# Kernel optimization log

Hardware: AMD Instinct MI355X
Metric: run time of the kernel (lower is better)

The kernel has to match this reference:

```python
import jax, jax.numpy as jnp
import numpy as np

B, L = 8, 1024
D_IN = 80 * 4          # input_feature_size * num_temporal_dimension_reduction_steps
CODE_DIM = 512         # code_book_size (projection dim)
NUM_CODES = 8192       # num_code_books (entries argmin'd over)


def setup_inputs() -> dict:
    key = jax.random.key(0)
    k1, k2, k3 = jax.random.split(key, 3)
    input_values = jax.random.normal(k1, (B, L, D_IN), dtype=jnp.float32)
    # all-ones mask keeps N = B*L static (jit-friendly); math identical to mask==1 selection
    mask_time_indices = jnp.ones((B, L), dtype=jnp.int32)
    # xavier_uniform for Linear weight of shape (out=CODE_DIM, in=D_IN)
    limit = float(np.sqrt(6.0 / (D_IN + CODE_DIM)))
    proj_weight = jax.random.uniform(k2, (CODE_DIM, D_IN), dtype=jnp.float32,
                                     minval=-limit, maxval=limit)
    code_book = jax.random.normal(k3, (NUM_CODES, CODE_DIM), dtype=jnp.float32)
    return {"input_values": input_values, "mask_time_indices": mask_time_indices,
            "proj_weight": proj_weight, "code_book": code_book}


def reference(input_values, mask_time_indices, proj_weight, code_book):
    D = input_values.shape[-1]
    flat = input_values.reshape(-1, D)                       # (B*L, D)
    sel = flat[mask_time_indices.reshape(-1) == 1]           # (N, D) masked tokens
    targets = sel @ proj_weight.T                            # (N, CODE_DIM)
    # squared euclidean distance via GEMM expansion: ||t||^2 - 2 t.c + ||c||^2
    t2 = jnp.sum(targets * targets, axis=-1, keepdims=True)  # (N, 1)
    c2 = jnp.sum(code_book * code_book, axis=-1)             # (NUM_CODES,)
    d2 = t2 - 2.0 * (targets @ code_book.T) + c2             # (N, NUM_CODES)
    # argmin of squared distance == argmin of euclidean norm
    return jnp.argmin(d2, axis=-1)                           # (N,)
```

## Files before the change

kernel.cpp:

```cpp
#include <hip/hip_runtime.h>


#define D_IN      320
#define CODE_DIM  512
#define NUM_CODES 8192
#define N_ROWS    8192

typedef _Float16 f16;
typedef __attribute__((ext_vector_type(4))) _Float16 f16x4;
typedef __attribute__((ext_vector_type(8))) _Float16 f16x8;
typedef __attribute__((ext_vector_type(4))) float    f32x4;

__global__ __launch_bounds__(256) void c2_kernel(const float* __restrict__ cb,
                                                 float* __restrict__ c2) {
    int wave = (blockIdx.x * blockDim.x + threadIdx.x) >> 6;
    int lane = threadIdx.x & 63;
    if (wave >= NUM_CODES) return;
    const float* row = cb + (size_t)wave * CODE_DIM;
    float s = 0.f;
#pragma unroll
    for (int i = 0; i < CODE_DIM / 64; ++i) {
        float v = row[lane + 64 * i];
        s += v * v;
    }
#pragma unroll
    for (int off = 32; off > 0; off >>= 1) s += __shfl_down(s, off, 64);
    if (lane == 0) c2[wave] = s;
}

__global__ __launch_bounds__(256) void cvt_kernel(const float* __restrict__ src,
                                                  f16* __restrict__ hi,
                                                  f16* __restrict__ lo, int n4) {
    int i = blockIdx.x * blockDim.x + threadIdx.x;
    if (i >= n4) return;
    float4 v = ((const float4*)src)[i];
    f16 h0 = (f16)v.x, h1 = (f16)v.y, h2 = (f16)v.z, h3 = (f16)v.w;
    f16x4 hv = {h0, h1, h2, h3};
    f16x4 lv = {(f16)(v.x - (float)h0), (f16)(v.y - (float)h1),
                (f16)(v.z - (float)h2), (f16)(v.w - (float)h3)};
    *(f16x4*)&hi[(size_t)i * 4] = hv;
    *(f16x4*)&lo[(size_t)i * 4] = lv;
}

#define PB_M 64
#define PB_N 64
#define PB_K 32
#define PLD  (PB_K + 4)

__global__ __launch_bounds__(256) void proj_kernel(const float* __restrict__ X,
                                                   const float* __restrict__ W,
                                                   f16* __restrict__ Thi,
                                                   f16* __restrict__ Tlo) {
    __shared__ float Xs[PB_M][PLD];
    __shared__ float Wsh[PB_N][PLD];
    const int bm = blockIdx.x;
    const int bn = blockIdx.y;
    const int tid = threadIdx.x;
    const int tx = tid & 15;
    const int ty = tid >> 4;
    float acc[4][4] = {};
    for (int kc = 0; kc < D_IN; kc += PB_K) {
#pragma unroll
        for (int it = 0; it < 2; ++it) {
            int idx = tid + 256 * it;
            int r   = idx >> 3;
            int kp  = (idx & 7) * 4;
            *(float4*)&Xs[r][kp] =
                *(const float4*)(X + (size_t)(bm * PB_M + r) * D_IN + kc + kp);
            *(float4*)&Wsh[r][kp] =
                *(const float4*)(W + (size_t)(bn * PB_N + r) * D_IN + kc + kp);
        }
        __syncthreads();
#pragma unroll
        for (int kk = 0; kk < PB_K; ++kk) {
            float a[4], b[4];
#pragma unroll
            for (int i = 0; i < 4; ++i) a[i] = Xs[ty + 16 * i][kk];
#pragma unroll
            for (int j = 0; j < 4; ++j) b[j] = Wsh[tx + 16 * j][kk];
#pragma unroll
            for (int i = 0; i < 4; ++i)
#pragma unroll
                for (int j = 0; j < 4; ++j) acc[i][j] += a[i] * b[j];
        }
        __syncthreads();
    }
#pragma unroll
    for (int i = 0; i < 4; ++i)
#pragma unroll
        for (int j = 0; j < 4; ++j) {
            size_t idx = (size_t)(bm * PB_M + ty + 16 * i) * CODE_DIM +
                         bn * PB_N + tx + 16 * j;
            float v = acc[i][j];
            f16  h = (f16)v;
            Thi[idx] = h;
            Tlo[idx] = (f16)(v - (float)h);
        }
}

#define BM 128
#define BN 128
#define BK 64

__global__ __launch_bounds__(256) void dist_mfma_kernel(
        const f16* __restrict__ Thi, const f16* __restrict__ Tlo,
        const f16* __restrict__ Chi, const f16* __restrict__ Clo,
        const float* __restrict__ c2, float2* __restrict__ part) {
    __shared__ f16 Ah[BM * BK], Al[BM * BK];
    __shared__ f16 Bh[BN * BK], Bl[BN * BK];
    __shared__ float red_v[BM][2];
    __shared__ int   red_i[BM][2];

    const int tid = threadIdx.x;
    const int l   = tid & 63;
    const int w   = tid >> 6;
    const int wr  = w >> 1;
    const int wc  = w & 1;
    const int rb  = blockIdx.y * BM;
    const int cbase = blockIdx.x * BN;

    f32x4 acc[4][4];
#pragma unroll
    for (int i = 0; i < 4; ++i)
#pragma unroll
        for (int j = 0; j < 4; ++j) acc[i][j] = (f32x4){0.f, 0.f, 0.f, 0.f};

    for (int kc = 0; kc < CODE_DIM; kc += BK) {
        __syncthreads();
#pragma unroll
        for (int it = 0; it < 4; ++it) {
            int idx = tid + 256 * it;
            int r   = idx >> 3;
            int kp  = (idx & 7) * 8;
            int db  = r * 128 + ((kp * 2) ^ ((r & 7) << 4));
            size_t ga = (size_t)(rb + r) * CODE_DIM + kc + kp;
            size_t gb = (size_t)(cbase + r) * CODE_DIM + kc + kp;
            *(uint4*)((char*)Ah + db) = *(const uint4*)(Thi + ga);
            *(uint4*)((char*)Al + db) = *(const uint4*)(Tlo + ga);
            *(uint4*)((char*)Bh + db) = *(const uint4*)(Chi + gb);
            *(uint4*)((char*)Bl + db) = *(const uint4*)(Clo + gb);
        }
        __syncthreads();
#pragma unroll
        for (int ks = 0; ks < 2; ++ks) {
            const int kb = ks * 64 + (l >> 4) * 16;
            f16x8 ah[4], al[4], bh[4], bl[4];
#pragma unroll
            for (int i = 0; i < 4; ++i) {
                int r   = wr * 64 + i * 16 + (l & 15);
                int off = r * 128 + (kb ^ ((r & 7) << 4));
                ah[i] = *(const f16x8*)((const char*)Ah + off);
                al[i] = *(const f16x8*)((const char*)Al + off);
            }
#pragma unroll
            for (int j = 0; j < 4; ++j) {
                int c   = wc * 64 + j * 16 + (l & 15);
                int off = c * 128 + (kb ^ ((c & 7) << 4));
                bh[j] = *(const f16x8*)((const char*)Bh + off);
                bl[j] = *(const f16x8*)((const char*)Bl + off);
            }
#pragma unroll
            for (int i = 0; i < 4; ++i)
#pragma unroll
                for (int j = 0; j < 4; ++j) {
                    acc[i][j] = __builtin_amdgcn_mfma_f32_16x16x32_f16(
                        ah[i], bh[j], acc[i][j], 0, 0, 0);
                    acc[i][j] = __builtin_amdgcn_mfma_f32_16x16x32_f16(
                        ah[i], bl[j], acc[i][j], 0, 0, 0);
                    acc[i][j] = __builtin_amdgcn_mfma_f32_16x16x32_f16(
                        al[i], bh[j], acc[i][j], 0, 0, 0);
                }
        }
    }

#pragma unroll
    for (int i = 0; i < 4; ++i) {
        float bvv[4];
        int   bii[4];
#pragma unroll
        for (int p = 0; p < 4; ++p) { bvv[p] = 3.4e38f; bii[p] = 0x7fffffff; }
#pragma unroll
        for (int j = 0; j < 4; ++j) {
            int   code = cbase + wc * 64 + j * 16 + (l & 15);
            float cc   = c2[code];
#pragma unroll
            for (int p = 0; p < 4; ++p) {
                float s = cc - 2.0f * acc[i][j][p];
                if (s < bvv[p]) { bvv[p] = s; bii[p] = code; }
            }
        }
#pragma unroll
        for (int off = 1; off < 16; off <<= 1) {
#pragma unroll
            for (int p = 0; p < 4; ++p) {
                float ov = __shfl_xor(bvv[p], off, 64);
                int   oi = __shfl_xor(bii[p], off, 64);
                if (ov < bvv[p] || (ov == bvv[p] && oi < bii[p])) {
                    bvv[p] = ov; bii[p] = oi;
                }
            }
        }
        if ((l & 15) == 0) {
#pragma unroll
            for (int p = 0; p < 4; ++p) {
                int rloc = wr * 64 + i * 16 + (l >> 4) * 4 + p;
                red_v[rloc][wc] = bvv[p];
                red_i[rloc][wc] = bii[p];
            }
        }
    }
    __syncthreads();
    if (tid < BM) {
        float v0 = red_v[tid][0], v1 = red_v[tid][1];
        int   i0 = red_i[tid][0], i1 = red_i[tid][1];
        bool  t1 = (v1 < v0) || (v1 == v0 && i1 < i0);
        part[(size_t)(rb + tid) * (NUM_CODES / BN) + blockIdx.x] =
            make_float2(t1 ? v1 : v0, __int_as_float(t1 ? i1 : i0));
    }
}

__global__ __launch_bounds__(256) void argmin_reduce_kernel(
        const float2* __restrict__ part, int* __restrict__ out) {
    int row  = blockIdx.x * 4 + (threadIdx.x >> 6);
    int lane = threadIdx.x & 63;
    float2 p = part[(size_t)row * 64 + lane];
    float bv = p.x;
    int   bi = __float_as_int(p.y);
#pragma unroll
    for (int off = 32; off > 0; off >>= 1) {
        float ov = __shfl_down(bv, off, 64);
        int   oi = __shfl_down(bi, off, 64);
        if (ov < bv || (ov == bv && oi < bi)) { bv = ov; bi = oi; }
    }
    if (lane == 0) out[row] = bi;
}

extern "C" void kernel_launch(void* const* d_in, const int* in_sizes, int n_in,
                              void* d_out, int out_size, void* d_ws, size_t ws_size,
                              hipStream_t stream) {
    const float* X  = (const float*)d_in[0];
    const float* W  = (const float*)d_in[2];
    const float* CB = (const float*)d_in[3];
    int* out = (int*)d_out;

    const size_t PLANE = (size_t)N_ROWS * CODE_DIM * sizeof(f16);
    char* ws = (char*)d_ws;
    f16*    Thi = (f16*)(ws);
    f16*    Tlo = (f16*)(ws + PLANE);
    f16*    Chi = (f16*)(ws + 2 * PLANE);
    f16*    Clo = (f16*)(ws + 3 * PLANE);
    float*  c2  = (float*)(ws + 4 * PLANE);
    float2* part = (float2*)(ws + 4 * PLANE + NUM_CODES * sizeof(float));

    c2_kernel<<<NUM_CODES / 4, 256, 0, stream>>>(CB, c2);

    cvt_kernel<<<(NUM_CODES * CODE_DIM / 4) / 256, 256, 0, stream>>>(
        CB, Chi, Clo, NUM_CODES * CODE_DIM / 4);

    dim3 pgrid(N_ROWS / PB_M, CODE_DIM / PB_N);
    proj_kernel<<<pgrid, 256, 0, stream>>>(X, W, Thi, Tlo);

    dim3 dgrid(NUM_CODES / BN, N_ROWS / BM);
    dist_mfma_kernel<<<dgrid, 256, 0, stream>>>(Thi, Tlo, Chi, Clo, c2, part);

    argmin_reduce_kernel<<<N_ROWS / 4, 256, 0, stream>>>(part, out);
}
```

Measured before the change: 351.3 us.

## Fuse codebook norm with fp16 split and halve LDS K-tile in distance GEMM

Merges the codebook squared-norm kernel and the fp16 hi/lo conversion kernel into one pass, so the codebook is read once and one launch is dropped. The distance GEMM K-tile shrinks from 64 to 32 and hi/lo planes are packed into one shared uint4 buffer with an XOR swizzle, halving LDS use per block to allow more resident blocks. The cost is twice as many K iterations and barriers per tile, with less MFMA work between syncs and no double buffering.

```diff
diff --git a/kernel.cpp b/kernel.cpp
--- a/kernel.cpp
+++ b/kernel.cpp
@@ -11,35 +11,31 @@
 typedef __attribute__((ext_vector_type(8))) _Float16 f16x8;
 typedef __attribute__((ext_vector_type(4))) float    f32x4;
 
-__global__ __launch_bounds__(256) void c2_kernel(const float* __restrict__ cb,
-                                                 float* __restrict__ c2) {
-    int wave = (blockIdx.x * blockDim.x + threadIdx.x) >> 6;
+__global__ __launch_bounds__(256) void c2cvt_kernel(const float* __restrict__ cb,
+                                                    float* __restrict__ c2,
+                                                    f16* __restrict__ hi,
+                                                    f16* __restrict__ lo) {
+    int wave = blockIdx.x * 4 + (threadIdx.x >> 6);
     int lane = threadIdx.x & 63;
-    if (wave >= NUM_CODES) return;
     const float* row = cb + (size_t)wave * CODE_DIM;
+    float4 v0 = *(const float4*)(row + lane * 8);
+    float4 v1 = *(const float4*)(row + lane * 8 + 4);
+    float vv[8] = {v0.x, v0.y, v0.z, v0.w, v1.x, v1.y, v1.z, v1.w};
+    f16x8 hv, lv;
     float s = 0.f;
 #pragma unroll
-    for (int i = 0; i < CODE_DIM / 64; ++i) {
-        float v = row[lane + 64 * i];
+    for (int i = 0; i < 8; ++i) {
+        float v = vv[i];
         s += v * v;
-    }
+        f16 h = (f16)v;
+        hv[i] = h;
+        lv[i] = (f16)(v - (float)h);
+    }
+    *(f16x8*)(hi + (size_t)wave * CODE_DIM + lane * 8) = hv;
+    *(f16x8*)(lo + (size_t)wave * CODE_DIM + lane * 8) = lv;
 #pragma unroll
     for (int off = 32; off > 0; off >>= 1) s += __shfl_down(s, off, 64);
     if (lane == 0) c2[wave] = s;
-}
-
-__global__ __launch_bounds__(256) void cvt_kernel(const float* __restrict__ src,
-                                                  f16* __restrict__ hi,
-                                                  f16* __restrict__ lo, int n4) {
-    int i = blockIdx.x * blockDim.x + threadIdx.x;
-    if (i >= n4) return;
-    float4 v = ((const float4*)src)[i];
-    f16 h0 = (f16)v.x, h1 = (f16)v.y, h2 = (f16)v.z, h3 = (f16)v.w;
-    f16x4 hv = {h0, h1, h2, h3};
-    f16x4 lv = {(f16)(v.x - (float)h0), (f16)(v.y - (float)h1),
-                (f16)(v.z - (float)h2), (f16)(v.w - (float)h3)};
-    *(f16x4*)&hi[(size_t)i * 4] = hv;
-    *(f16x4*)&lo[(size_t)i * 4] = lv;
 }
 
 #define PB_M 64
@@ -100,14 +96,13 @@
 
 #define BM 128
 #define BN 128
-#define BK 64
+#define BK 32
 
 __global__ __launch_bounds__(256) void dist_mfma_kernel(
         const f16* __restrict__ Thi, const f16* __restrict__ Tlo,
         const f16* __restrict__ Chi, const f16* __restrict__ Clo,
         const float* __restrict__ c2, float2* __restrict__ part) {
-    __shared__ f16 Ah[BM * BK], Al[BM * BK];
-    __shared__ f16 Bh[BN * BK], Bl[BN * BK];
+    __shared__ uint4 lds4[2048];
     __shared__ float red_v[BM][2];
     __shared__ int   red_i[BM][2];
 
@@ -118,6 +113,7 @@
     const int wc  = w & 1;
     const int rb  = blockIdx.y * BM;
     const int cbase = blockIdx.x * BN;
+    const int cgrp = l >> 4;
 
     f32x4 acc[4][4];
 #pragma unroll
@@ -128,49 +124,45 @@
     for (int kc = 0; kc < CODE_DIM; kc += BK) {
         __syncthreads();
 #pragma unroll
-        for (int it = 0; it < 4; ++it) {
-            int idx = tid + 256 * it;
-            int r   = idx >> 3;
-            int kp  = (idx & 7) * 8;
-            int db  = r * 128 + ((kp * 2) ^ ((r & 7) << 4));
-            size_t ga = (size_t)(rb + r) * CODE_DIM + kc + kp;
-            size_t gb = (size_t)(cbase + r) * CODE_DIM + kc + kp;
-            *(uint4*)((char*)Ah + db) = *(const uint4*)(Thi + ga);
-            *(uint4*)((char*)Al + db) = *(const uint4*)(Tlo + ga);
-            *(uint4*)((char*)Bh + db) = *(const uint4*)(Chi + gb);
-            *(uint4*)((char*)Bl + db) = *(const uint4*)(Clo + gb);
-        }
-        __syncthreads();
-#pragma unroll
-        for (int ks = 0; ks < 2; ++ks) {
-            const int kb = ks * 64 + (l >> 4) * 16;
-            f16x8 ah[4], al[4], bh[4], bl[4];
-#pragma unroll
-            for (int i = 0; i < 4; ++i) {
-                int r   = wr * 64 + i * 16 + (l & 15);
-                int off = r * 128 + (kb ^ ((r & 7) << 4));
-                ah[i] = *(const f16x8*)((const char*)Ah + off);
-                al[i] = *(const f16x8*)((const char*)Al + off);
-            }
+        for (int it = 0; it < 8; ++it) {
+            int slot = it * 256 + tid;
+            int mat  = slot >> 10;
+            int sm   = slot & 1023;
+            int r    = sm >> 3;
+            int c    = sm & 7;
+            const f16* src = mat ? (c < 4 ? Chi : Clo) : (c < 4 ? Thi : Tlo);
+            int row_g = (mat ? cbase : rb) + r;
+            uint4 v = *(const uint4*)(src + (size_t)row_g * CODE_DIM + kc +
+                                      (c & 3) * 8);
+            lds4[(mat << 10) + (r << 3) + (c ^ (r & 7))] = v;
+        }
+        __syncthreads();
+        f16x8 ah[4], al[4], bh[4], bl[4];
+#pragma unroll
+        for (int i = 0; i < 4; ++i) {
+            int r = wr * 64 + i * 16 + (l & 15);
+            int s = r & 7;
+            ah[i] = *(const f16x8*)&lds4[(r << 3) + (cgrp ^ s)];
+            al[i] = *(const f16x8*)&lds4[(r << 3) + ((4 + cgrp) ^ s)];
+        }
+#pragma unroll
+        for (int j = 0; j < 4; ++j) {
+            int r = wc * 64 + j * 16 + (l & 15);
+            int s = r & 7;
+            bh[j] = *(const f16x8*)&lds4[1024 + (r << 3) + (cgrp ^ s)];
+            bl[j] = *(const f16x8*)&lds4[1024 + (r << 3) + ((4 + cgrp) ^ s)];
+        }
+#pragma unroll
+        for (int i = 0; i < 4; ++i)
 #pragma unroll
             for (int j = 0; j < 4; ++j) {
-                int c   = wc * 64 + j * 16 + (l & 15);
-                int off = c * 128 + (kb ^ ((c & 7) << 4));
-                bh[j] = *(const f16x8*)((const char*)Bh + off);
-                bl[j] = *(const f16x8*)((const char*)Bl + off);
-            }
-#pragma unroll
-            for (int i = 0; i < 4; ++i)
-#pragma unroll
-                for (int j = 0; j < 4; ++j) {
-                    acc[i][j] = __builtin_amdgcn_mfma_f32_16x16x32_f16(
-                        ah[i], bh[j], acc[i][j], 0, 0, 0);
-                    acc[i][j] = __builtin_amdgcn_mfma_f32_16x16x32_f16(
-                        ah[i], bl[j], acc[i][j], 0, 0, 0);
-                    acc[i][j] = __builtin_amdgcn_mfma_f32_16x16x32_f16(
-                        al[i], bh[j], acc[i][j], 0, 0, 0);
-                }
-        }
+                acc[i][j] = __builtin_amdgcn_mfma_f32_16x16x32_f16(
+                    ah[i], bh[j], acc[i][j], 0, 0, 0);
+                acc[i][j] = __builtin_amdgcn_mfma_f32_16x16x32_f16(
+                    ah[i], bl[j], acc[i][j], 0, 0, 0);
+                acc[i][j] = __builtin_amdgcn_mfma_f32_16x16x32_f16(
+                    al[i], bh[j], acc[i][j], 0, 0, 0);
+            }
     }
 
 #pragma unroll
@@ -252,10 +244,7 @@
     float*  c2  = (float*)(ws + 4 * PLANE);
     float2* part = (float2*)(ws + 4 * PLANE + NUM_CODES * sizeof(float));
 
-    c2_kernel<<<NUM_CODES / 4, 256, 0, stream>>>(CB, c2);
-
-    cvt_kernel<<<(NUM_CODES * CODE_DIM / 4) / 256, 256, 0, stream>>>(
-        CB, Chi, Clo, NUM_CODES * CODE_DIM / 4);
+    c2cvt_kernel<<<NUM_CODES / 4, 256, 0, stream>>>(CB, c2, Chi, Clo);
 
     dim3 pgrid(N_ROWS / PB_M, CODE_DIM / PB_N);
     proj_kernel<<<pgrid, 256, 0, stream>>>(X, W, Thi, Tlo);
```

Result: slower. 377.4 us (+7.4%).
